# Performance work log

Hardware: AMD Instinct MI355X
Metric: run time of the kernel (lower is better)

The kernel has to match this reference:

```python
import jax, jax.numpy as jnp
import numpy as np

B, T, DIM, MC = 64, 128, 768, 30  # batch, seq len, input_dim, middle_channel


def _cdist(a, b):
    # torch.cdist(a, b, p=2): [B,T,d] x [B,T,d] -> [B,T,T]
    sq = (jnp.sum(a * a, -1)[:, :, None] + jnp.sum(b * b, -1)[:, None, :]
          - 2.0 * jnp.einsum('bid,bjd->bij', a, b))
    return jnp.sqrt(jnp.clip(sq, 1e-12))


def _conv(x, w, b):
    # NCHW 'same' conv, stride 1
    y = jax.lax.conv_general_dilated(x, w, (1, 1), 'SAME',
                                     dimension_numbers=('NCHW', 'OIHW', 'NCHW'))
    return y + b[None, :, None, None]


def setup_inputs() -> dict:
    key = jax.random.key(0)
    ks = jax.random.split(key, 10)
    q_seq = jax.random.normal(ks[0], (B, T, DIM), jnp.float32)
    k_seq = jax.random.normal(ks[1], (B, T, DIM), jnp.float32)
    q_len_seq = jax.random.randint(ks[2], (B, 1), 1, T + 1).astype(jnp.int32)
    k_len_seq = jax.random.randint(ks[3], (B, 1), 1, T + 1).astype(jnp.int32)
    q_R = jax.random.uniform(ks[4], (B, T), jnp.float32)
    k_R = jax.random.uniform(ks[5], (B, T), jnp.float32)
    conv1_w = jax.random.normal(ks[6], (MC, 2, 5, 5), jnp.float32) * 0.05
    conv2_w = jax.random.normal(ks[7], (MC, MC, 5, 5), jnp.float32) * 0.02
    conv3_w = jax.random.normal(ks[8], (1, MC, 3, 3), jnp.float32) * 0.05
    conv1_b = jnp.zeros((MC,), jnp.float32)
    conv2_b = jnp.zeros((MC,), jnp.float32)
    conv3_b = jnp.zeros((1,), jnp.float32)
    return dict(q_seq=q_seq, q_len_seq=q_len_seq, q_R=q_R,
                k_seq=k_seq, k_len_seq=k_len_seq, k_R=k_R,
                conv1_w=conv1_w, conv1_b=conv1_b,
                conv2_w=conv2_w, conv2_b=conv2_b,
                conv3_w=conv3_w, conv3_b=conv3_b)


def reference(q_seq, q_len_seq, q_R, k_seq, k_len_seq, k_R,
              conv1_w, conv1_b, conv2_w, conv2_b, conv3_w, conv3_b):
    bsz = q_seq.shape[0]
    Tq = q_seq.shape[1]
    D = _cdist(q_seq, k_seq)                                  # [B,T,T]
    P = jnp.abs(q_R[:, :, None] - k_R[:, None, :])            # cdist on 1-d R
    pos = jnp.arange(Tq, dtype=jnp.int32)
    row_mask = pos[None, :] < q_len_seq                       # [B,T]
    col_mask = pos[None, :] < k_len_seq                       # [B,T]
    mask = row_mask[:, :, None] & col_mask[:, None, :]        # [B,T,T]
    maskf = mask.astype(D.dtype)
    D = D * maskf
    P = P * maskf
    A = jnp.stack([D, P], axis=1)                             # [B,2,T,T]
    A = jax.nn.relu(_conv(A, conv1_w, conv1_b))
    A = jax.nn.relu(_conv(A, conv2_w, conv2_b))
    A = _conv(A, conv3_w, conv3_b)[:, 0] + D                  # [B,T,T]
    A = jnp.where(mask, A, jnp.float32(100.0))
    A = jax.nn.softmax(-A, axis=2)
    At = A.reshape(bsz, Tq * Tq)
    At = At / jnp.sum(jnp.abs(At), axis=1, keepdims=True)     # L1 normalize
    dis = jnp.einsum('bn,bn->b', D.reshape(bsz, Tq * Tq), At)
    return (A, dis)
```

## Files before the change

### kernel.cpp

```cpp
#include <hip/hip_runtime.h>
#include <hip/hip_bf16.h>
#include <stdint.h>

using u16 = unsigned short;
using u32 = unsigned int;
using u8  = unsigned char;

#define NB 64
#define TT 128
#define DK 768
#define MC 30

typedef float f32x16 __attribute__((ext_vector_type(16)));
typedef __bf16 bf16x8 __attribute__((ext_vector_type(8)));
typedef long long ll;
typedef __attribute__((ext_vector_type(2))) ll ll2;
#if __has_builtin(__builtin_amdgcn_mfma_scale_f32_32x32x64_f8f6f4)
#define HAVE_MXFP8 1
typedef int i32x8 __attribute__((ext_vector_type(8)));
#endif
#if __has_builtin(__builtin_amdgcn_global_load_lds)
#define HAVE_GLDS 1
#endif

__device__ inline void unpack2(u32 u, float& lo, float& hi){
  union{u32 i; float f;} a, b; a.i = u << 16; b.i = u & 0xFFFF0000u; lo = a.f; hi = b.f;
}
__device__ inline u16 f2bf(float f){
  union{u32 i; float f;} v; v.f = f;
  u32 r = v.i + 0x7FFFu + ((v.i >> 16) & 1u);
  return (u16)(r >> 16);
}
__device__ inline u32 pack2bf(float a, float b){ return (u32)f2bf(a) | ((u32)f2bf(b) << 16); }

#if __has_builtin(__builtin_amdgcn_cvt_pk_fp8_f32)
template<bool HIW>
__device__ inline u32 pk_fp8(float a, float b, u32 old){
  return (u32)__builtin_amdgcn_cvt_pk_fp8_f32(a, b, (int)old, HIW);
}
#else
__device__ inline u8 f2fp8_1(float f){
  union{float f; u32 u;} v; v.f = f;
  u32 s = (v.u >> 24) & 0x80u;
  u32 abs = v.u & 0x7fffffffu;
  if (abs < 0x3c800000u){
    float sc = fabsf(f) * 512.0f;
    int m = (int)rintf(sc);
    return (u8)(s | (u32)m);
  }
  u32 e8 = abs >> 23; u32 mant = abs & 0x7fffffu;
  u32 m3 = mant >> 20; u32 rest = mant & 0xfffffu;
  u32 rb = (rest > 0x80000u) || (rest == 0x80000u && (m3 & 1u));
  m3 += rb;
  u32 E = e8 - 120u;
  if (m3 == 8u){ m3 = 0u; E += 1u; }
  if (E >= 16u || (E == 15u && m3 == 7u)) return (u8)(s | 0x7Eu);
  return (u8)(s | (E << 3) | m3);
}
template<bool HIW>
__device__ inline u32 pk_fp8(float a, float b, u32 old){
  u32 w = (u32)f2fp8_1(a) | ((u32)f2fp8_1(b) << 8);
  return HIW ? ((old & 0x0000FFFFu) | (w << 16)) : ((old & 0xFFFF0000u) | w);
}
#endif

#if __has_builtin(__builtin_amdgcn_cvt_pk_f32_fp8)
__device__ inline void upk_fp8x4(u32 w, float* x){
  auto a0 = __builtin_amdgcn_cvt_pk_f32_fp8((int)w, false);
  auto a1 = __builtin_amdgcn_cvt_pk_f32_fp8((int)w, true);
  x[0] = a0[0]; x[1] = a0[1]; x[2] = a1[0]; x[3] = a1[1];
}
#else
__device__ inline float fp8_1(u32 byte){
  u32 s = (byte & 0x80u) << 24;
  u32 E = (byte >> 3) & 15u, M = byte & 7u;
  union{u32 u; float f;} v;
  if (E == 0){ v.f = (float)M * (1.0f/512.0f); v.u |= s; }
  else v.u = s | ((E + 120u) << 23) | (M << 20);
  return v.f;
}
__device__ inline void upk_fp8x4(u32 w, float* x){
  x[0] = fp8_1(w & 255u); x[1] = fp8_1((w >> 8) & 255u);
  x[2] = fp8_1((w >> 16) & 255u); x[3] = fp8_1(w >> 24);
}
#endif

__global__ __launch_bounds__(256) void prep_w_k(const float* __restrict__ w2,
    const float* __restrict__ w1, u8* __restrict__ w2p, u16* __restrict__ w1c){
  int bidx = blockIdx.x;
  if (bidx < 25){
    int tap = bidx;
    int i = threadIdx.x;
    int oc = i >> 3, q = i & 7, ic0 = q * 4;
    float v[4];
    #pragma unroll
    for (int j = 0; j < 4; ++j)
      v[j] = (oc < MC && ic0 + j < MC) ? w2[(oc*MC + ic0 + j)*25 + tap] : 0.f;
    u32 w = pk_fp8<false>(v[0], v[1], 0u);
    w = pk_fp8<true>(v[2], v[3], w);
    int lo = ((oc << 5) + (q << 2)) ^ ((oc & 7) << 4);
    *(u32*)(w2p + tap*1024 + lo) = w;
  } else {
    for (int i = threadIdx.x; i < 2560; i += 256){
      int dy = i >> 9; int rem = i & 511; int oc = rem >> 4; int k = rem & 15;
      int dx = k >> 1, c = k & 1;
      float v = (oc < MC && dx < 5) ? w1[(oc*2 + c)*25 + dy*5 + dx] : 0.f;
      int byteoff = dy*1024 + (((oc<<5) + (k<<1)) ^ ((oc&7)<<4));
      *(u16*)((char*)w1c + byteoff) = f2bf(v);
    }
  }
}

__global__ __launch_bounds__(256) void row_norms_k(const float* __restrict__ q, const float* __restrict__ k,
    float* __restrict__ qq, float* __restrict__ kk,
    u16* __restrict__ qb16, u16* __restrict__ kb16){
  int wave = blockIdx.x * 4 + (threadIdx.x >> 6);
  int lane = threadIdx.x & 63;
  const float* src; float* dst; u16* bdst; int row;
  if (wave < NB * TT) { src = q; dst = qq; bdst = qb16; row = wave; }
  else                { src = k; dst = kk; bdst = kb16; row = wave - NB * TT; }
  const float4* p = (const float4*)(src + (size_t)row * DK);
  char* ob = (char*)(bdst + (size_t)row * DK);
  int key = (row & 7) << 4;
  float s = 0.f;
  {
    float4 a = p[2*lane], b2 = p[2*lane + 1];
    s += a.x*a.x + a.y*a.y + a.z*a.z + a.w*a.w;
    s += b2.x*b2.x + b2.y*b2.y + b2.z*b2.z + b2.w*b2.w;
    uint4 st;
    st.x = pack2bf(a.x, a.y);  st.y = pack2bf(a.z, a.w);
    st.z = pack2bf(b2.x, b2.y); st.w = pack2bf(b2.z, b2.w);
    *(uint4*)(ob + ((lane << 4) ^ key)) = st;
  }
  if (lane < 32){
    int g = 64 + lane;
    float4 a = p[2*g], b2 = p[2*g + 1];
    s += a.x*a.x + a.y*a.y + a.z*a.z + a.w*a.w;
    s += b2.x*b2.x + b2.y*b2.y + b2.z*b2.z + b2.w*b2.w;
    uint4 st;
    st.x = pack2bf(a.x, a.y);  st.y = pack2bf(a.z, a.w);
    st.z = pack2bf(b2.x, b2.y); st.w = pack2bf(b2.z, b2.w);
    *(uint4*)(ob + ((g << 4) ^ key)) = st;
  }
  #pragma unroll
  for (int o = 32; o; o >>= 1) s += __shfl_xor(s, o);
  if (lane == 0) dst[row] = s;
}

__global__ __launch_bounds__(256) void cdist_mfma_k(
    const u16* __restrict__ Qb16, const u16* __restrict__ Kb16,
    const float* __restrict__ qq, const float* __restrict__ kk,
    const int* __restrict__ qlen, const int* __restrict__ klen,
    const float* __restrict__ qR, const float* __restrict__ kR,
    float* __restrict__ Dout, u32* __restrict__ inb){
  __shared__ __align__(16) char qs[32 * 1536];
  __shared__ __align__(16) char ksm[128 * 256];
  int bid = blockIdx.x;
  int b  = ((bid & 7) << 3) + (bid >> 5);
  int rt = (bid >> 3) & 3;
  int r0 = rt * 32;
  int tid = threadIdx.x;
  int lane = tid & 63, w = tid >> 6;
  int hi = lane >> 5, l31 = lane & 31;
  const char* Qg = (const char*)(Qb16 + ((size_t)b * TT + r0) * DK);
  const char* Kg = (const char*)(Kb16 + (size_t)b * TT * DK);
#ifdef HAVE_GLDS
  #pragma unroll
  for (int i = 0; i < 12; ++i){
    int gb = (i*4 + w) << 6;
    __builtin_amdgcn_global_load_lds((const u32*)(Qg + ((gb + lane) << 4)),
                                     (u32*)(qs + (gb << 4)), 16, 0, 0);
  }
#else
  for (int idx = tid; idx < 3072; idx += 256)
    *(uint4*)(qs + idx*16) = *(const uint4*)(Qg + idx*16);
#endif
  int col = w * 32 + l31;
  f32x16 acc;
  #pragma unroll
  for (int r = 0; r < 16; ++r) acc[r] = 0.f;
  for (int kc = 0; kc < DK; kc += 128){
    __syncthreads();
#ifdef HAVE_GLDS
    const char* Ks = Kg + kc*2;
    #pragma unroll
    for (int i = 0; i < 8; ++i){
      int gb = (i*4 + w) << 6;
      int g = gb + lane;
      __builtin_amdgcn_global_load_lds((const u32*)(Ks + (g >> 4)*1536 + ((g & 15) << 4)),
                                       (u32*)(ksm + (gb << 4)), 16, 0, 0);
    }
#else
    for (int idx = tid; idx < 2048; idx += 256){
      int c = idx >> 4, j = idx & 15;
      *(uint4*)(ksm + idx*16) = *(const uint4*)(Kg + c*1536 + kc*2 + j*16);
    }
#endif
    __syncthreads();
    #pragma unroll
    for (int k8 = 0; k8 < 8; ++k8){
      bf16x8 a  = *(const bf16x8*)(qs  + l31 * 1536 + (((kc + k8*16 + hi*8) * 2) ^ ((l31 & 7) << 4)));
      bf16x8 bv = *(const bf16x8*)(ksm + col * 256  + (((k8*16 + hi*8) * 2) ^ ((col & 7) << 4)));
      acc = __builtin_amdgcn_mfma_f32_32x32x16_bf16(a, bv, acc, 0, 0, 0);
    }
  }
  int ql = qlen[b], kl = klen[b];
  float kkv = kk[b * TT + col];
  float krv = kR[b * TT + col];
  bool cm = col < kl;
  #pragma unroll
  for (int r = 0; r < 16; ++r){
    int row = r0 + (r & 3) + 8 * (r >> 2) + 4 * hi;
    float qqv = qq[b * TT + row];
    float sq = qqv + kkv - 2.f * acc[r];
    float d = sqrtf(fmaxf(sq, 1e-12f));
    bool m = (row < ql) && cm;
    float dm = m ? d : 0.f;
    float pm = m ? fabsf(qR[b * TT + row] - krv) : 0.f;
    Dout[(((size_t)b * TT + row) << 7) + col] = dm;
    inb[(((size_t)b * TT + row) << 7) + col] = pack2bf(dm, pm);
  }
}

#define C1_ROWW 136
#define C2_IN_ROWB 4224
#define F_INB_BYTES (16*C1_ROWW*4)
#define F_C2_OFF F_INB_BYTES
#define F_SMEM (F_INB_BYTES + 12*C2_IN_ROWB)

__global__ __launch_bounds__(512, 4) void conv12_mfma_k(
    const u32* __restrict__ inb, const u8* __restrict__ w2p, const u16* __restrict__ w1c,
    const float* __restrict__ b1, const float* __restrict__ b2, u8* __restrict__ act2){
  __shared__ __align__(16) char smem[F_SMEM];
  u32* ilds = (u32*)smem;
  char* c2in = smem + F_C2_OFF;
  int o  = blockIdx.x;
  int yg = ((o & 7) << 1) + (o >> 3);
  int bb = blockIdx.y;
  int y0 = yg * 8;
  int tid = threadIdx.x;
  for (int i = tid; i < 16*C1_ROWW; i += 512){
    int r = i / C1_ROWW, xi = i - r * C1_ROWW;
    int gy = y0 - 4 + r, gx = xi - 2;
    u32 v = 0;
    if ((unsigned)gy < 128u && (unsigned)gx < 128u)
      v = inb[(((size_t)bb * 128 + gy) << 7) + gx];
    ilds[r * C1_ROWW + xi] = v;
  }
  for (int i = tid; i < 96; i += 512){
    int r = i >> 3; int rem = i & 7; int ci = rem >> 1; int h = rem & 1;
    int lx = (ci < 2) ? ci : (128 + ci);
    int addr = r*C2_IN_ROWB + (((lx << 5) + (h << 4)) ^ ((lx & 7) << 4));
    *(uint4*)(c2in + addr) = make_uint4(0,0,0,0);
  }
  int lane = tid & 63, w = tid >> 6;
  int hi = lane >> 5, l31 = lane & 31;
  int aSwz = ((l31 << 5) + (hi << 4)) ^ ((l31 & 7) << 4);
  bf16x8 afr[5];
  #pragma unroll
  for (int dy = 0; dy < 5; ++dy)
    afr[dy] = *(const bf16x8*)((const char*)w1c + dy*1024 + aSwz);
  float b1v[16];
  #pragma unroll
  for (int r = 0; r < 16; ++r){
    int oc = (r & 3) + 8*(r >> 2) + 4*hi;
    b1v[r] = (oc < MC) ? b1[oc] : 0.f;
  }
  __syncthreads();
  for (int rep = 0; rep < 2; ++rep){
    if (rep == 1 && w >= 4) break;
    int idx = (rep == 0) ? w : (8 + w);
    int gy = y0 - 2 + idx;
    bool oob = (unsigned)gy >= 128u;
    #pragma unroll
    for (int t = 0; t < 4; ++t){
      int px = t*32 + l31;
      u32 words[4];
      if (!oob){
        f32x16 acc;
        #pragma unroll
        for (int r = 0; r < 16; ++r) acc[r] = 0.f;
        #pragma unroll
        for (int dy = 0; dy < 5; ++dy){
          const u32* rp = &ilds[(idx + dy)*C1_ROWW + px + hi*4];
          union { u32 uw[4]; bf16x8 v; } ub;
          ub.uw[0] = rp[0]; ub.uw[1] = rp[1]; ub.uw[2] = rp[2]; ub.uw[3] = rp[3];
          acc = __builtin_amdgcn_mfma_f32_32x32x16_bf16(afr[dy], ub.v, acc, 0, 0, 0);
        }
        #pragma unroll
        for (int q = 0; q < 4; ++q){
          u32 word = pk_fp8<false>(fmaxf(acc[4*q+0]+b1v[4*q+0], 0.f),
                                   fmaxf(acc[4*q+1]+b1v[4*q+1], 0.f), 0u);
          word = pk_fp8<true>(fmaxf(acc[4*q+2]+b1v[4*q+2], 0.f),
                              fmaxf(acc[4*q+3]+b1v[4*q+3], 0.f), word);
          words[q] = word;
        }
      } else {
        words[0] = words[1] = words[2] = words[3] = 0u;
      }
      int lx = px + 2;
      #pragma unroll
      for (int q = 0; q < 4; ++q){
        int ic = q*8 + hi*4;
        int addr = idx*C2_IN_ROWB + (((lx << 5) + ic) ^ ((lx & 7) << 4));
        *(u32*)(c2in + addr) = words[q];
      }
    }
  }
  __syncthreads();
  f32x16 acc[4];
  #pragma unroll
  for (int t = 0; t < 4; ++t)
    #pragma unroll
    for (int r = 0; r < 16; ++r) acc[t][r] = 0.f;
  #pragma unroll
  for (int dy = 0; dy < 5; ++dy){
    const char* rowp = c2in + (w + dy)*C2_IN_ROWB;
    ll2 aw[5];
    #pragma unroll
    for (int dx = 0; dx < 5; ++dx)
      aw[dx] = *(const ll2*)(w2p + (dy*5 + dx)*1024 + aSwz);
#ifdef HAVE_MXFP8
    union U8x { struct { ll2 lo, hi; } p; i32x8 v; };
    U8x a01, a23, a4z;
    ll2 zz; zz.x = 0; zz.y = 0;
    a01.p.lo = aw[0]; a01.p.hi = aw[1];
    a23.p.lo = aw[2]; a23.p.hi = aw[3];
    a4z.p.lo = aw[4]; a4z.p.hi = zz;
    #pragma unroll
    for (int t = 0; t < 4; ++t){
      int pxb = t*32 + l31;
      ll2 bl[5];
      #pragma unroll
      for (int dx = 0; dx < 5; ++dx){
        int px2 = pxb + dx;
        int boff = ((px2 << 5) + (hi << 4)) ^ ((px2 & 7) << 4);
        bl[dx] = *(const ll2*)(rowp + boff);
      }
      U8x b01, b23, b4d;
      b01.p.lo = bl[0]; b01.p.hi = bl[1];
      b23.p.lo = bl[2]; b23.p.hi = bl[3];
      b4d.p.lo = bl[4]; b4d.p.hi = bl[4];
      acc[t] = __builtin_amdgcn_mfma_scale_f32_32x32x64_f8f6f4(
                 a01.v, b01.v, acc[t], 0, 0, 0, 0x7F7F7F7F, 0, 0x7F7F7F7F);
      acc[t] = __builtin_amdgcn_mfma_scale_f32_32x32x64_f8f6f4(
                 a23.v, b23.v, acc[t], 0, 0, 0, 0x7F7F7F7F, 0, 0x7F7F7F7F);
      acc[t] = __builtin_amdgcn_mfma_scale_f32_32x32x64_f8f6f4(
                 a4z.v, b4d.v, acc[t], 0, 0, 0, 0x7F7F7F7F, 0, 0x7F7F7F7F);
    }
#else
    #pragma unroll
    for (int dx = 0; dx < 5; ++dx){
      ll2 a = aw[dx];
      #pragma unroll
      for (int t = 0; t < 4; ++t){
        int px2 = t*32 + l31 + dx;
        int boff = ((px2 << 5) + (hi << 4)) ^ ((px2 & 7) << 4);
        ll2 b = *(const ll2*)(rowp + boff);
        acc[t] = __builtin_amdgcn_mfma_f32_32x32x16_fp8_fp8(a.x, b.x, acc[t], 0, 0, 0);
        acc[t] = __builtin_amdgcn_mfma_f32_32x32x16_fp8_fp8(a.y, b.y, acc[t], 0, 0, 0);
      }
    }
#endif
  }
  float b2v[16];
  #pragma unroll
  for (int r = 0; r < 16; ++r){
    int oc = (r & 3) + 8*(r >> 2) + 4*hi;
    b2v[r] = (oc < MC) ? b2[oc] : 0.f;
  }
  __syncthreads();
  int wbase = w * 4096;
  #pragma unroll
  for (int t = 0; t < 4; ++t){
    int px = t*32 + l31;
    #pragma unroll
    for (int q = 0; q < 4; ++q){
      float v0 = fmaxf(acc[t][4*q+0] + b2v[4*q+0], 0.f);
      float v1 = fmaxf(acc[t][4*q+1] + b2v[4*q+1], 0.f);
      float v2 = fmaxf(acc[t][4*q+2] + b2v[4*q+2], 0.f);
      float v3 = fmaxf(acc[t][4*q+3] + b2v[4*q+3], 0.f);
      u32 word = pk_fp8<false>(v0, v1, 0u);
      word = pk_fp8<true>(v2, v3, word);
      int addr = wbase + (((px<<5) + (q<<3) + (hi<<2)) ^ (((px>>2)&3)<<3));
      *(u32*)(c2in + addr) = word;
    }
  }
  int y = y0 + w;
  #pragma unroll
  for (int p = 0; p < 8; ++p){
    int x = p*16 + (lane >> 2), cg = lane & 3;
    int addr = wbase + (((x<<5) + (cg<<3)) ^ (((x>>2)&3)<<3));
    uint2 v = *(const uint2*)(c2in + addr);
    *(uint2*)(act2 + ((((size_t)bb*128 + y)*128 + x) << 5) + cg*8) = v;
  }
}

__global__ __launch_bounds__(512) void conv3sm_k(const u8* __restrict__ act2,
    const float* __restrict__ w3, const float* __restrict__ b3, const float* __restrict__ Dbuf,
    const int* __restrict__ qlen, const int* __restrict__ klen,
    float* __restrict__ Aout, float* __restrict__ rowsum, int b0){
  __shared__ float wlds[9][32];
  __shared__ float ex0[512], ex2[512];
  __shared__ float redm[8], reds[8], redd[8];
  int o  = blockIdx.x;
  int ip = ((o & 7) << 3) + (o >> 3);
  int bb = blockIdx.y;
  int b  = b0 + bb;
  int tid = threadIdx.x;
  for (int idx = tid; idx < 288; idx += 512){
    int tap = idx >> 5, c = idx & 31;
    wlds[tap][c] = (c < MC) ? w3[c * 9 + tap] : 0.f;
  }
  __syncthreads();
  int r  = tid >> 8;
  int t  = tid & 255;
  int px = t >> 1, half = t & 1;
  int i  = ip * 2 + r;
  int wv = tid >> 6;
  float T0 = 0.f, T1 = 0.f, T2 = 0.f;
  #pragma unroll
  for (int dy = 0; dy < 3; ++dy){
    int gy = i - 1 + dy;
    uint4 v = make_uint4(0, 0, 0, 0);
    if ((unsigned)gy < 128u)
      v = *(const uint4*)(act2 + ((((size_t)bb*128 + gy)*128 + px) << 5) + half*16);
    float x[16];
    upk_fp8x4(v.x, x); upk_fp8x4(v.y, x + 4);
    upk_fp8x4(v.z, x + 8); upk_fp8x4(v.w, x + 12);
    const float* w0p = &wlds[dy*3 + 0][half*16];
    const float* w1p = &wlds[dy*3 + 1][half*16];
    const float* w2q = &wlds[dy*3 + 2][half*16];
    #pragma unroll
    for (int c = 0; c < 16; ++c){
      T0 = fmaf(x[c], w0p[c], T0);
      T1 = fmaf(x[c], w1p[c], T1);
      T2 = fmaf(x[c], w2q[c], T2);
    }
  }
  ex0[tid] = T0; ex2[tid] = T2;
  __syncthreads();
  float acc = T1;
  if (px > 0)   acc += ex0[tid - 2];
  if (px < 127) acc += ex2[tid + 2];
  acc += __shfl_xor(acc, 1);
  acc += b3[0];
  float Dv = Dbuf[(((size_t)b * 128 + i) << 7) + px];
  bool m = (i < qlen[b]) && (px < klen[b]);
  float xv = m ? -(acc + Dv) : -100.f;
  float mx = xv;
  #pragma unroll
  for (int o2 = 32; o2; o2 >>= 1) mx = fmaxf(mx, __shfl_xor(mx, o2));
  if ((tid & 63) == 0) redm[wv] = mx;
  __syncthreads();
  int rb4 = r << 2;
  mx = fmaxf(fmaxf(redm[rb4], redm[rb4+1]), fmaxf(redm[rb4+2], redm[rb4+3]));
  float e = __expf(xv - mx);
  float s  = e;
  float de = Dv * e;
  #pragma unroll
  for (int o2 = 32; o2; o2 >>= 1){ s += __shfl_xor(s, o2); de += __shfl_xor(de, o2); }
  if ((tid & 63) == 0){ reds[wv] = s; redd[wv] = de; }
  __syncthreads();
  float s4 = (reds[rb4] + reds[rb4+1]) + (reds[rb4+2] + reds[rb4+3]);
  float a = e * 2.0f / s4;
  if (half == 0) Aout[(((size_t)b * 128 + i) << 7) + px] = a;
  if (t == 0){
    float d4 = (redd[rb4] + redd[rb4+1]) + (redd[rb4+2] + redd[rb4+3]);
    rowsum[b * TT + i] = d4 / s4;
  }
}

__global__ __launch_bounds__(128) void dis_k(const float* __restrict__ rowsum, float* __restrict__ out){
  int b = blockIdx.x, tid = threadIdx.x;
  float v = rowsum[b * TT + tid];
  #pragma unroll
  for (int o = 32; o; o >>= 1) v += __shfl_xor(v, o);
  __shared__ float red[2];
  if ((tid & 63) == 0) red[tid >> 6] = v;
  __syncthreads();
  if (tid == 0) out[b] = (red[0] + red[1]) * (1.0f / 128.0f);
}

extern "C" void kernel_launch(void* const* d_in, const int* in_sizes, int n_in,
                              void* d_out, int out_size, void* d_ws, size_t ws_size,
                              hipStream_t stream){
  const float* q_seq = (const float*)d_in[0];
  const int*   q_len = (const int*)d_in[1];
  const float* q_R   = (const float*)d_in[2];
  const float* k_seq = (const float*)d_in[3];
  const int*   k_len = (const int*)d_in[4];
  const float* k_R   = (const float*)d_in[5];
  const float* c1w   = (const float*)d_in[6];
  const float* c1b   = (const float*)d_in[7];
  const float* c2w   = (const float*)d_in[8];
  const float* c2b   = (const float*)d_in[9];
  const float* c3w   = (const float*)d_in[10];
  const float* c3b   = (const float*)d_in[11];
  float* out = (float*)d_out;

  char* base = (char*)d_ws;
  size_t off = 0;
  auto take = [&](size_t bytes)->char*{
    char* p = base + off;
    off = (off + bytes + 255) & ~(size_t)255;
    return p;
  };
  float* Dbuf   = (float*)take((size_t)NB * TT * TT * 4);
  float* qq     = (float*)take((size_t)NB * TT * 4);
  float* kkn    = (float*)take((size_t)NB * TT * 4);
  float* rowsum = (float*)take((size_t)NB * TT * 4);
  u32*   inb    = (u32*)  take((size_t)NB * TT * TT * 4);
  u8*    w2p    = (u8*)   take(25 * 1024);
  u16*   w1c    = (u16*)  take(5 * 1024);
  u16*   qb16   = (u16*)  take((size_t)NB * TT * DK * 2);
  u16*   kb16   = (u16*)  take((size_t)NB * TT * DK * 2);
  size_t fixed = off;
  int BCH = 64;
  while (BCH > 1 && fixed + (size_t)BCH * TT * TT * 32 + 1024 > ws_size) BCH >>= 1;
  u8* act2 = (u8*)take((size_t)BCH * TT * TT * 32);

  prep_w_k<<<26, 256, 0, stream>>>(c2w, c1w, w2p, w1c);
  row_norms_k<<<4096, 256, 0, stream>>>(q_seq, k_seq, qq, kkn, qb16, kb16);
  cdist_mfma_k<<<256, 256, 0, stream>>>(qb16, kb16, qq, kkn, q_len, k_len, q_R, k_R, Dbuf, inb);
  for (int b0 = 0; b0 < NB; b0 += BCH){
    int nb = BCH;
    conv12_mfma_k<<<dim3(16, nb), 512, 0, stream>>>(inb + (size_t)b0 * TT * TT, w2p, w1c, c1b, c2b, act2);
    conv3sm_k<<<dim3(64, nb), 512, 0, stream>>>(act2, c3w, c3b, Dbuf, q_len, k_len, out, rowsum, b0);
  }
  dis_k<<<NB, 128, 0, stream>>>(rowsum, out + (size_t)NB * TT * TT);
}
```

Baseline: 98.53 us.

## Split conv1+conv2 fused tiles into half-width column tiles

The fused conv1/conv2 kernel now processes an 8-row by 64-column tile instead of a full 128-wide row band, launching twice as many blocks with about half the shared memory each. Conv1 is computed over a 68-column haloed strip with out-of-range columns zeroed, replacing the explicit edge zero-padding pass. This aims at more blocks in flight and smaller LDS per block. The trade-off is redundant halo computation and wasted MFMA lanes in the third conv1 column tile.

```diff
diff --git a/kernel.cpp b/kernel.cpp
--- a/kernel.cpp
+++ b/kernel.cpp
@@ -222,36 +222,32 @@
   }
 }
 
-#define C1_ROWW 136
-#define C2_IN_ROWB 4224
-#define F_INB_BYTES (16*C1_ROWW*4)
-#define F_C2_OFF F_INB_BYTES
-#define F_SMEM (F_INB_BYTES + 12*C2_IN_ROWB)
+#define C1H_ROWW 72
+#define C2H_ROWB 2176
+#define FH_INB_BYTES (16*C1H_ROWW*4)
+#define FH_C2_OFF FH_INB_BYTES
+#define FH_SMEM (FH_INB_BYTES + 12*C2H_ROWB)
 
 __global__ __launch_bounds__(512, 4) void conv12_mfma_k(
     const u32* __restrict__ inb, const u8* __restrict__ w2p, const u16* __restrict__ w1c,
     const float* __restrict__ b1, const float* __restrict__ b2, u8* __restrict__ act2){
-  __shared__ __align__(16) char smem[F_SMEM];
+  __shared__ __align__(16) char smem[FH_SMEM];
   u32* ilds = (u32*)smem;
-  char* c2in = smem + F_C2_OFF;
+  char* c2in = smem + FH_C2_OFF;
   int o  = blockIdx.x;
-  int yg = ((o & 7) << 1) + (o >> 3);
+  int tI = ((o & 7) << 2) + (o >> 3);
+  int yg = tI >> 1, xh = tI & 1;
   int bb = blockIdx.y;
   int y0 = yg * 8;
+  int x0 = xh * 64;
   int tid = threadIdx.x;
-  for (int i = tid; i < 16*C1_ROWW; i += 512){
-    int r = i / C1_ROWW, xi = i - r * C1_ROWW;
-    int gy = y0 - 4 + r, gx = xi - 2;
+  for (int i = tid; i < 16*C1H_ROWW; i += 512){
+    int r = i / C1H_ROWW, xi = i - r * C1H_ROWW;
+    int gy = y0 - 4 + r, gx = x0 - 4 + xi;
     u32 v = 0;
     if ((unsigned)gy < 128u && (unsigned)gx < 128u)
       v = inb[(((size_t)bb * 128 + gy) << 7) + gx];
-    ilds[r * C1_ROWW + xi] = v;
-  }
-  for (int i = tid; i < 96; i += 512){
-    int r = i >> 3; int rem = i & 7; int ci = rem >> 1; int h = rem & 1;
-    int lx = (ci < 2) ? ci : (128 + ci);
-    int addr = r*C2_IN_ROWB + (((lx << 5) + (h << 4)) ^ ((lx & 7) << 4));
-    *(uint4*)(c2in + addr) = make_uint4(0,0,0,0);
+    ilds[r * C1H_ROWW + xi] = v;
   }
   int lane = tid & 63, w = tid >> 6;
   int hi = lane >> 5, l31 = lane & 31;
@@ -271,51 +267,49 @@
     if (rep == 1 && w >= 4) break;
     int idx = (rep == 0) ? w : (8 + w);
     int gy = y0 - 2 + idx;
-    bool oob = (unsigned)gy >= 128u;
-    #pragma unroll
-    for (int t = 0; t < 4; ++t){
-      int px = t*32 + l31;
-      u32 words[4];
-      if (!oob){
-        f32x16 acc;
-        #pragma unroll
-        for (int r = 0; r < 16; ++r) acc[r] = 0.f;
-        #pragma unroll
-        for (int dy = 0; dy < 5; ++dy){
-          const u32* rp = &ilds[(idx + dy)*C1_ROWW + px + hi*4];
-          union { u32 uw[4]; bf16x8 v; } ub;
-          ub.uw[0] = rp[0]; ub.uw[1] = rp[1]; ub.uw[2] = rp[2]; ub.uw[3] = rp[3];
-          acc = __builtin_amdgcn_mfma_f32_32x32x16_bf16(afr[dy], ub.v, acc, 0, 0, 0);
-        }
+    bool oobRow = (unsigned)gy >= 128u;
+    #pragma unroll
+    for (int t = 0; t < 3; ++t){
+      int j  = t*32 + l31;
+      int jr = (j < 67) ? j : 67;
+      int gx = x0 - 2 + j;
+      bool valid = !oobRow && ((unsigned)gx < 128u);
+      f32x16 acc;
+      #pragma unroll
+      for (int r = 0; r < 16; ++r) acc[r] = 0.f;
+      #pragma unroll
+      for (int dy = 0; dy < 5; ++dy){
+        const u32* rp = &ilds[(idx + dy)*C1H_ROWW + jr + hi*4];
+        union { u32 uw[4]; bf16x8 v; } ub;
+        ub.uw[0] = rp[0]; ub.uw[1] = rp[1]; ub.uw[2] = rp[2]; ub.uw[3] = rp[3];
+        acc = __builtin_amdgcn_mfma_f32_32x32x16_bf16(afr[dy], ub.v, acc, 0, 0, 0);
+      }
+      if (j < 68){
         #pragma unroll
         for (int q = 0; q < 4; ++q){
-          u32 word = pk_fp8<false>(fmaxf(acc[4*q+0]+b1v[4*q+0], 0.f),
-                                   fmaxf(acc[4*q+1]+b1v[4*q+1], 0.f), 0u);
-          word = pk_fp8<true>(fmaxf(acc[4*q+2]+b1v[4*q+2], 0.f),
-                              fmaxf(acc[4*q+3]+b1v[4*q+3], 0.f), word);
-          words[q] = word;
+          u32 word = 0u;
+          if (valid){
+            word = pk_fp8<false>(fmaxf(acc[4*q+0]+b1v[4*q+0], 0.f),
+                                 fmaxf(acc[4*q+1]+b1v[4*q+1], 0.f), 0u);
+            word = pk_fp8<true>(fmaxf(acc[4*q+2]+b1v[4*q+2], 0.f),
+                                fmaxf(acc[4*q+3]+b1v[4*q+3], 0.f), word);
+          }
+          int ic = q*8 + hi*4;
+          int addr = idx*C2H_ROWB + (((j << 5) + ic) ^ ((j & 7) << 4));
+          *(u32*)(c2in + addr) = word;
         }
-      } else {
-        words[0] = words[1] = words[2] = words[3] = 0u;
       }
-      int lx = px + 2;
-      #pragma unroll
-      for (int q = 0; q < 4; ++q){
-        int ic = q*8 + hi*4;
-        int addr = idx*C2_IN_ROWB + (((lx << 5) + ic) ^ ((lx & 7) << 4));
-        *(u32*)(c2in + addr) = words[q];
-      }
-    }
-  }
-  __syncthreads();
-  f32x16 acc[4];
-  #pragma unroll
-  for (int t = 0; t < 4; ++t)
+    }
+  }
+  __syncthreads();
+  f32x16 acc[2];
+  #pragma unroll
+  for (int t = 0; t < 2; ++t)
     #pragma unroll
     for (int r = 0; r < 16; ++r) acc[t][r] = 0.f;
   #pragma unroll
   for (int dy = 0; dy < 5; ++dy){
-    const char* rowp = c2in + (w + dy)*C2_IN_ROWB;
+    const char* rowp = c2in + (w + dy)*C2H_ROWB;
     ll2 aw[5];
     #pragma unroll
     for (int dx = 0; dx < 5; ++dx)
@@ -328,7 +322,7 @@
     a23.p.lo = aw[2]; a23.p.hi = aw[3];
     a4z.p.lo = aw[4]; a4z.p.hi = zz;
     #pragma unroll
-    for (int t = 0; t < 4; ++t){
+    for (int t = 0; t < 2; ++t){
       int pxb = t*32 + l31;
       ll2 bl[5];
       #pragma unroll
@@ -353,7 +347,7 @@
     for (int dx = 0; dx < 5; ++dx){
       ll2 a = aw[dx];
       #pragma unroll
-      for (int t = 0; t < 4; ++t){
+      for (int t = 0; t < 2; ++t){
         int px2 = t*32 + l31 + dx;
         int boff = ((px2 << 5) + (hi << 4)) ^ ((px2 & 7) << 4);
         ll2 b = *(const ll2*)(rowp + boff);
@@ -370,10 +364,10 @@
     b2v[r] = (oc < MC) ? b2[oc] : 0.f;
   }
   __syncthreads();
-  int wbase = w * 4096;
-  #pragma unroll
-  for (int t = 0; t < 4; ++t){
-    int px = t*32 + l31;
+  int wbase = w * 2048;
+  #pragma unroll
+  for (int t = 0; t < 2; ++t){
+    int p = t*32 + l31;
     #pragma unroll
     for (int q = 0; q < 4; ++q){
       float v0 = fmaxf(acc[t][4*q+0] + b2v[4*q+0], 0.f);
@@ -382,17 +376,17 @@
       float v3 = fmaxf(acc[t][4*q+3] + b2v[4*q+3], 0.f);
       u32 word = pk_fp8<false>(v0, v1, 0u);
       word = pk_fp8<true>(v2, v3, word);
-      int addr = wbase + (((px<<5) + (q<<3) + (hi<<2)) ^ (((px>>2)&3)<<3));
+      int addr = wbase + (((p<<5) + (q<<3) + (hi<<2)) ^ (((p>>2)&3)<<3));
       *(u32*)(c2in + addr) = word;
     }
   }
   int y = y0 + w;
   #pragma unroll
-  for (int p = 0; p < 8; ++p){
-    int x = p*16 + (lane >> 2), cg = lane & 3;
-    int addr = wbase + (((x<<5) + (cg<<3)) ^ (((x>>2)&3)<<3));
+  for (int pp = 0; pp < 4; ++pp){
+    int xl = pp*16 + (lane >> 2), cg = lane & 3;
+    int addr = wbase + (((xl<<5) + (cg<<3)) ^ (((xl>>2)&3)<<3));
     uint2 v = *(const uint2*)(c2in + addr);
-    *(uint2*)(act2 + ((((size_t)bb*128 + y)*128 + x) << 5) + cg*8) = v;
+    *(uint2*)(act2 + ((((size_t)bb*128 + y)*128 + x0 + xl) << 5) + cg*8) = v;
   }
 }
 
@@ -525,7 +519,7 @@
   cdist_mfma_k<<<256, 256, 0, stream>>>(qb16, kb16, qq, kkn, q_len, k_len, q_R, k_R, Dbuf, inb);
   for (int b0 = 0; b0 < NB; b0 += BCH){
     int nb = BCH;
-    conv12_mfma_k<<<dim3(16, nb), 512, 0, stream>>>(inb + (size_t)b0 * TT * TT, w2p, w1c, c1b, c2b, act2);
+    conv12_mfma_k<<<dim3(32, nb), 512, 0, stream>>>(inb + (size_t)b0 * TT * TT, w2p, w1c, c1b, c2b, act2);
     conv3sm_k<<<dim3(64, nb), 512, 0, stream>>>(act2, c3w, c3b, Dbuf, q_len, k_len, out, rowsum, b0);
   }
   dis_k<<<NB, 128, 0, stream>>>(rowsum, out + (size_t)NB * TT * TT);
```

New measurement: 106.1 us. 1.08x slower.
